# Kernel tuning notes

Hardware: AMD Instinct MI355X
Metric: run time of the kernel (lower is better)

Reference implementation:

```python
import jax, jax.numpy as jnp
import numpy as np

N = 100000   # nodes
E = 1600000  # edges (before self-loops)
F = 128      # num_features
H = 128      # hidden_dim
EPS = 1e-5   # BatchNorm eps


def setup_inputs() -> dict:
    key = jax.random.key(0)
    ks = jax.random.split(key, 8)
    x = jax.random.normal(ks[0], (N, F), dtype=jnp.float32)
    edge_index = jax.random.randint(ks[1], (2, E), 0, N, dtype=jnp.int64)

    def lin(k, din, dout):
        s = 1.0 / np.sqrt(din)
        kw, kb = jax.random.split(k)
        W = jax.random.uniform(kw, (din, dout), jnp.float32, -s, s)
        b = jax.random.uniform(kb, (dout,), jnp.float32, -s, s)
        return W, b

    W1, b1 = lin(ks[2], F, H)
    W2, b2 = lin(ks[3], H, H)
    W3, b3 = lin(ks[4], H, H)
    Wc, bc = lin(ks[5], H, 2)

    def bn_params():
        return (jnp.ones((H,), jnp.float32), jnp.zeros((H,), jnp.float32),
                jnp.zeros((H,), jnp.float32), jnp.ones((H,), jnp.float32))

    g1, be1, rm1, rv1 = bn_params()
    g2, be2, rm2, rv2 = bn_params()
    g3, be3, rm3, rv3 = bn_params()

    return {"x": x, "edge_index": edge_index,
            "W1": W1, "b1": b1, "W2": W2, "b2": b2, "W3": W3, "b3": b3,
            "g1": g1, "be1": be1, "rm1": rm1, "rv1": rv1,
            "g2": g2, "be2": be2, "rm2": rm2, "rv2": rv2,
            "g3": g3, "be3": be3, "rm3": rm3, "rv3": rv3,
            "Wc": Wc, "bc": bc}


def _gcn_norm(edge_index, num_nodes):
    # add self-loops, compute symmetric normalization (PyG GCNConv default)
    loop = jnp.arange(num_nodes, dtype=edge_index.dtype)
    src = jnp.concatenate([edge_index[0], loop])
    dst = jnp.concatenate([edge_index[1], loop])
    deg = jax.ops.segment_sum(jnp.ones_like(dst, dtype=jnp.float32), dst,
                              num_segments=num_nodes)
    dinv = jnp.where(deg > 0, jax.lax.rsqrt(deg), 0.0)
    norm = dinv[src] * dinv[dst]  # [E+N]
    return src, dst, norm


def _gcn_conv(x, W, b, src, dst, norm, num_nodes):
    h = x @ W                              # [N, H] linear first
    msg = h[src] * norm[:, None]           # gather + scale  [E+N, H]
    out = jax.ops.segment_sum(msg, dst, num_segments=num_nodes)  # scatter-add
    return out + b


def _bn_eval(x, g, be, rm, rv):
    return (x - rm) * jax.lax.rsqrt(rv + EPS) * g + be


def reference(x, edge_index,
              W1, b1, W2, b2, W3, b3,
              g1, be1, rm1, rv1,
              g2, be2, rm2, rv2,
              g3, be3, rm3, rv3,
              Wc, bc):
    n = x.shape[0]
    src, dst, norm = _gcn_norm(edge_index, n)
    h = _gcn_conv(x, W1, b1, src, dst, norm, n)
    h = _bn_eval(jax.nn.relu(h), g1, be1, rm1, rv1)
    # dropout: identity in eval mode
    h = _gcn_conv(h, W2, b2, src, dst, norm, n)
    h = _bn_eval(jax.nn.relu(h), g2, be2, rm2, rv2)
    h = _gcn_conv(h, W3, b3, src, dst, norm, n)
    h = _bn_eval(jax.nn.relu(h), g3, be3, rm3, rv3)
    return h @ Wc + bc  # [N, 2]
```

## Files before the change

kernel.cpp:

```cpp
#include <hip/hip_runtime.h>
#include <hip/hip_fp16.h>

#define BN_EPS 1e-5f
#define CHUNK 8192
#define BBITS 9

typedef _Float16 half8 __attribute__((ext_vector_type(8)));
typedef float f32x4 __attribute__((ext_vector_type(4)));

__device__ __forceinline__ float4 f4zero() { return make_float4(0.f, 0.f, 0.f, 0.f); }


__global__ __launch_bounds__(1024) void k_pack_hist(const float* __restrict__ W1,
                                                    const float* __restrict__ W2,
                                                    const float* __restrict__ W3,
                                                    _Float16* __restrict__ pW,
                                                    const int* __restrict__ dst,
                                                    int* __restrict__ tableT,
                                                    int nA, int nbuck, int e) {
    __shared__ int h[256];
    int tid = threadIdx.x;
    if (blockIdx.x < 6) {
        int t = blockIdx.x * 1024 + tid;
        int wi = t >> 11;
        int tt = t & 2047;
        const float* W = (wi == 0) ? W1 : ((wi == 1) ? W2 : W3);
        int kc = tt >> 9;
        int rem = tt & 511;
        int ct = rem >> 6;
        int lane = rem & 63;
        int q = lane >> 4;
        int col = ct * 16 + (lane & 15);
        half8 hh;
#pragma unroll
        for (int j = 0; j < 8; ++j)
            hh[j] = (_Float16)W[(kc * 32 + q * 8 + j) * 128 + col];
        *(half8*)(pW + (size_t)t * 8) = hh;
        return;
    }
    int blk = blockIdx.x - 6;
    if (tid < 256) h[tid] = 0;
    __syncthreads();
    int base = blk * CHUNK;
    if (base + CHUNK <= e) {
        const int4* d4 = (const int4*)(dst + base);
#pragma unroll
        for (int t = 0; t < CHUNK / 4096; ++t) {
            int4 d = d4[t * 1024 + tid];
            atomicAdd(&h[d.x >> BBITS], 1);
            atomicAdd(&h[d.y >> BBITS], 1);
            atomicAdd(&h[d.z >> BBITS], 1);
            atomicAdd(&h[d.w >> BBITS], 1);
        }
    } else {
        for (int i = base + tid; i < e; i += 1024)
            atomicAdd(&h[dst[i] >> BBITS], 1);
    }
    __syncthreads();
    for (int k = tid; k < nbuck; k += 1024)
        tableT[(size_t)k * nA + blk] = h[k];
}


__global__ __launch_bounds__(1024) void k_scan_block(const int* __restrict__ in,
                                                     int* __restrict__ outp,
                                                     int* __restrict__ partials, int len) {
    __shared__ int s[1024];
    int t = threadIdx.x;
    int gid = blockIdx.x * 1024 + t;
    int v = (gid < len) ? in[gid] : 0;
    int x = v;
    s[t] = x;
    __syncthreads();
    for (int d = 1; d < 1024; d <<= 1) {
        int y = (t >= d) ? s[t - d] : 0;
        __syncthreads();
        x += y;
        s[t] = x;
        __syncthreads();
    }
    if (gid < len) outp[gid] = x - v;
    if (t == 1023) partials[blockIdx.x] = x;
}

__global__ __launch_bounds__(256) void k_scan_addp(int* __restrict__ data,
                                                   const int* __restrict__ partials, int len) {
    __shared__ int red[256];
    int tid = threadIdx.x;
    int K = blockIdx.x >> 2;
    int s = 0;
    for (int t = tid; t < K; t += 256) s += partials[t];
    red[tid] = s;
    __syncthreads();
    for (int d = 128; d > 0; d >>= 1) {
        if (tid < d) red[tid] += red[tid + d];
        __syncthreads();
    }
    int gid = blockIdx.x * 256 + tid;
    if (gid < len) data[gid] += red[0];
}


__global__ __launch_bounds__(1024) void k_scatter(const int* __restrict__ src,
                                                  const int* __restrict__ dst,
                                                  const int* __restrict__ tableT,
                                                  int2* __restrict__ bed,
                                                  int nA, int nbuck, int e) {
    __shared__ int cur[256];
    int blk = blockIdx.x, tid = threadIdx.x;
    for (int k = tid; k < nbuck; k += 1024)
        cur[k] = tableT[(size_t)k * nA + blk];
    __syncthreads();
    int base = blk * CHUNK;
    if (base + CHUNK <= e) {
        const int4* s4 = (const int4*)(src + base);
        const int4* d4 = (const int4*)(dst + base);
#pragma unroll
        for (int t = 0; t < CHUNK / 4096; ++t) {
            int4 s = s4[t * 1024 + tid];
            int4 d = d4[t * 1024 + tid];
            int p0 = atomicAdd(&cur[d.x >> BBITS], 1); bed[p0] = make_int2(s.x, d.x);
            int p1 = atomicAdd(&cur[d.y >> BBITS], 1); bed[p1] = make_int2(s.y, d.y);
            int p2 = atomicAdd(&cur[d.z >> BBITS], 1); bed[p2] = make_int2(s.z, d.z);
            int p3 = atomicAdd(&cur[d.w >> BBITS], 1); bed[p3] = make_int2(s.w, d.w);
        }
    } else {
        for (int i = base + tid; i < e; i += 1024) {
            int d = dst[i];
            int p = atomicAdd(&cur[d >> BBITS], 1);
            bed[p] = make_int2(src[i], d);
        }
    }
}


template <bool AF32, bool SCALE>
__device__ __forceinline__ void gemm_body(int bid, int tid, char* smem,
                                          const void* __restrict__ Av,
                                          const _Float16* __restrict__ pW,
                                          const float* __restrict__ dinv,
                                          uint4* __restrict__ C, int n) {
    uint4* sW = (uint4*)smem;
    {
        const uint4* gW = (const uint4*)pW;
#pragma unroll
        for (int i = 0; i < 8; ++i) sW[tid + 256 * i] = gW[tid + 256 * i];
    }
    __syncthreads();

    int wave = tid >> 6, lane = tid & 63;
    int quad = lane >> 4, l16 = lane & 15;
    int row0 = bid * 64 + wave * 16;
    int arow = row0 + l16;
    int arowc = (arow < n) ? arow : (n - 1);

    half8 af[4];
    if (AF32) {
        const float* A = (const float*)Av + (size_t)arowc * 128 + quad * 8;
#pragma unroll
        for (int kc = 0; kc < 4; ++kc) {
            float4 lo = *(const float4*)(A + kc * 32);
            float4 hi = *(const float4*)(A + kc * 32 + 4);
            half8 h;
            h[0] = (_Float16)lo.x; h[1] = (_Float16)lo.y;
            h[2] = (_Float16)lo.z; h[3] = (_Float16)lo.w;
            h[4] = (_Float16)hi.x; h[5] = (_Float16)hi.y;
            h[6] = (_Float16)hi.z; h[7] = (_Float16)hi.w;
            af[kc] = h;
        }
    } else {
        const _Float16* A = (const _Float16*)Av + (size_t)arowc * 128 + quad * 8;
#pragma unroll
        for (int kc = 0; kc < 4; ++kc)
            af[kc] = *(const half8*)(A + kc * 32);
    }

    f32x4 acc[8];
#pragma unroll
    for (int ct = 0; ct < 8; ++ct) acc[ct] = (f32x4){0.f, 0.f, 0.f, 0.f};

#pragma unroll
    for (int kc = 0; kc < 4; ++kc) {
#pragma unroll
        for (int ct = 0; ct < 8; ++ct) {
            half8 bf = *(half8*)&sW[(kc * 8 + ct) * 64 + lane];
            acc[ct] = __builtin_amdgcn_mfma_f32_16x16x32_f16(af[kc], bf, acc[ct], 0, 0, 0);
        }
    }

    __syncthreads();

    _Float16* eb = (_Float16*)smem + wave * 16 * 136;
    float dv[4];
#pragma unroll
    for (int r = 0; r < 4; ++r) {
        if (SCALE) {
            int rr = row0 + quad * 4 + r;
            dv[r] = dinv[(rr < n) ? rr : (n - 1)];
        } else dv[r] = 1.f;
    }
#pragma unroll
    for (int ct = 0; ct < 8; ++ct)
#pragma unroll
        for (int r = 0; r < 4; ++r)
            eb[(quad * 4 + r) * 136 + ct * 16 + l16] =
                (_Float16)(SCALE ? acc[ct][r] * dv[r] : acc[ct][r]);

#pragma unroll
    for (int i = 0; i < 4; ++i) {
        int linear = i * 64 + lane;
        int r = linear >> 4, c = linear & 15;
        uint4 v = *(uint4*)((char*)eb + r * 272 + c * 16);
        int row = row0 + r;
        if (row < n) C[(size_t)row * 16 + c] = v;
    }
}

__global__ __launch_bounds__(256) void k_gemm_mfma(const void* __restrict__ Av,
                                                   const _Float16* __restrict__ pW,
                                                   const float* __restrict__ dinv,
                                                   uint4* __restrict__ C, int n) {
    __shared__ char smem[32768];
    gemm_body<false, true>(blockIdx.x, threadIdx.x, smem, Av, pW, dinv, C, n);
}


__global__ __launch_bounds__(256) void k_rank_gemm1(const int2* __restrict__ bed,
                                                    const int* __restrict__ tableT,
                                                    int2* __restrict__ offs2,
                                                    int* __restrict__ er,
                                                    float* __restrict__ dinv,
                                                    unsigned int* __restrict__ pad0,
                                                    const float* __restrict__ x,
                                                    const _Float16* __restrict__ pW,
                                                    uint4* __restrict__ C,
                                                    int nA, int nbuck, int n, int e) {
    __shared__ char smem[32768];
    int tid = threadIdx.x;
    int b = blockIdx.x;
    if (b >= nbuck) {
        gemm_body<true, false>(b - nbuck, tid, smem, x, pW, nullptr, C, n);
        return;
    }
    int* lcnt = (int*)smem;
    int* loff = lcnt + 512;
    int* s    = loff + 512;
    if (b == 0) {
        if (tid < 64) pad0[tid] = 0u;
        if (tid == 0) dinv[n] = 0.f;
    }
    for (int k = tid; k < 512; k += 256) lcnt[k] = 0;
    __syncthreads();
    int start = tableT[(size_t)b * nA];
    int end = (b + 1 < nbuck) ? tableT[(size_t)(b + 1) * nA] : e;
    for (int i = start + tid; i < end; i += 256)
        atomicAdd(&lcnt[bed[i].y & 511], 1);
    __syncthreads();
    int t2 = tid * 2;
    int c0 = lcnt[t2], c1 = lcnt[t2 + 1];
    int p0 = (c0 + 7) & ~7, p1 = (c1 + 7) & ~7;
    int xsum = p0 + p1;
    s[tid] = xsum;
    __syncthreads();
    for (int d = 1; d < 256; d <<= 1) {
        int y = (tid >= d) ? s[tid - d] : 0;
        __syncthreads();
        xsum += y;
        s[tid] = xsum;
        __syncthreads();
    }
    int ebase = start + (b << 12);
    int base0 = xsum - p0 - p1;
    loff[t2] = base0;
    loff[t2 + 1] = base0 + p0;
    {
        int node = (b << BBITS) + t2;
        if (node < n) {
            int o = ebase + base0;
            offs2[node] = make_int2(o, o + p0);
            dinv[node] = rsqrtf((float)(c0 + 1));
            for (int j = c0; j < p0; ++j) er[o + j] = n << 8;
        }
        node = (b << BBITS) + t2 + 1;
        if (node < n) {
            int o = ebase + base0 + p0;
            offs2[node] = make_int2(o, o + p1);
            dinv[node] = rsqrtf((float)(c1 + 1));
            for (int j = c1; j < p1; ++j) er[o + j] = n << 8;
        }
    }
    __syncthreads();
    for (int k = tid; k < 512; k += 256) lcnt[k] = 0;
    __syncthreads();
    for (int i = start + tid; i < end; i += 256) {
        int2 q = bed[i];
        int l = q.y & 511;
        int r = atomicAdd(&lcnt[l], 1);
        er[ebase + loff[l] + r] = q.x << 8;
    }
}


__device__ __forceinline__ void acc_row4(float4& aL, float4& aH, uint4 q) {
    asm("v_fma_mix_f32 %0, %1, 1.0, %0 op_sel:[0,0,0] op_sel_hi:[1,0,0]" : "+v"(aL.x) : "v"(q.x));
    asm("v_fma_mix_f32 %0, %1, 1.0, %0 op_sel:[1,0,0] op_sel_hi:[1,0,0]" : "+v"(aL.y) : "v"(q.x));
    asm("v_fma_mix_f32 %0, %1, 1.0, %0 op_sel:[0,0,0] op_sel_hi:[1,0,0]" : "+v"(aL.z) : "v"(q.y));
    asm("v_fma_mix_f32 %0, %1, 1.0, %0 op_sel:[1,0,0] op_sel_hi:[1,0,0]" : "+v"(aL.w) : "v"(q.y));
    asm("v_fma_mix_f32 %0, %1, 1.0, %0 op_sel:[0,0,0] op_sel_hi:[1,0,0]" : "+v"(aH.x) : "v"(q.z));
    asm("v_fma_mix_f32 %0, %1, 1.0, %0 op_sel:[1,0,0] op_sel_hi:[1,0,0]" : "+v"(aH.y) : "v"(q.z));
    asm("v_fma_mix_f32 %0, %1, 1.0, %0 op_sel:[0,0,0] op_sel_hi:[1,0,0]" : "+v"(aH.z) : "v"(q.w));
    asm("v_fma_mix_f32 %0, %1, 1.0, %0 op_sel:[1,0,0] op_sel_hi:[1,0,0]" : "+v"(aH.w) : "v"(q.w));
}

__device__ __forceinline__ void acc_row4s(float4& aL, float4& aH, uint4 q, float s) {
    asm("v_fma_mix_f32 %0, %1, %2, %0 op_sel:[0,0,0] op_sel_hi:[1,0,0]" : "+v"(aL.x) : "v"(q.x), "v"(s));
    asm("v_fma_mix_f32 %0, %1, %2, %0 op_sel:[1,0,0] op_sel_hi:[1,0,0]" : "+v"(aL.y) : "v"(q.x), "v"(s));
    asm("v_fma_mix_f32 %0, %1, %2, %0 op_sel:[0,0,0] op_sel_hi:[1,0,0]" : "+v"(aL.z) : "v"(q.y), "v"(s));
    asm("v_fma_mix_f32 %0, %1, %2, %0 op_sel:[1,0,0] op_sel_hi:[1,0,0]" : "+v"(aL.w) : "v"(q.y), "v"(s));
    asm("v_fma_mix_f32 %0, %1, %2, %0 op_sel:[0,0,0] op_sel_hi:[1,0,0]" : "+v"(aH.x) : "v"(q.z), "v"(s));
    asm("v_fma_mix_f32 %0, %1, %2, %0 op_sel:[1,0,0] op_sel_hi:[1,0,0]" : "+v"(aH.y) : "v"(q.z), "v"(s));
    asm("v_fma_mix_f32 %0, %1, %2, %0 op_sel:[0,0,0] op_sel_hi:[1,0,0]" : "+v"(aH.z) : "v"(q.w), "v"(s));
    asm("v_fma_mix_f32 %0, %1, %2, %0 op_sel:[1,0,0] op_sel_hi:[1,0,0]" : "+v"(aH.w) : "v"(q.w), "v"(s));
}


template <bool FUSE_CLS, bool SRC_SCALE>
__global__ __launch_bounds__(256) void k_aggregate(const uint4* __restrict__ Ah,
                                                   const int2* __restrict__ offs2,
                                                   const int* __restrict__ er,
                                                   const float* __restrict__ dinv,
                                                   const float* __restrict__ bias,
                                                   const float* __restrict__ g,
                                                   const float* __restrict__ be,
                                                   const float* __restrict__ rm,
                                                   const float* __restrict__ rv,
                                                   uint4* __restrict__ Hout,
                                                   const float* __restrict__ Wc,
                                                   const float* __restrict__ bc,
                                                   float* __restrict__ out, int n) {
    int lane = threadIdx.x & 15;
    int node = blockIdx.x * 16 + (threadIdx.x >> 4);
    if (node >= n) return;

    const char* AhB = (const char*)Ah;
    unsigned int l16b = (unsigned int)lane * 16u;

    float di = dinv[node];
    float4 aL = f4zero(), aH = f4zero();
    {
        uint4 qs = *(const uint4*)(AhB + (((unsigned int)node << 8) + l16b));
        if (SRC_SCALE) acc_row4s(aL, aH, qs, di);
        else           acc_row4(aL, aH, qs);
    }

    int2 offc = offs2[node];
    for (int e = offc.x; e < offc.y; e += 8) {
        int4 ra = *(const int4*)(er + e);
        int4 rb = *(const int4*)(er + e + 4);
        uint4 v0 = *(const uint4*)(AhB + ((unsigned int)ra.x + l16b));
        uint4 v1 = *(const uint4*)(AhB + ((unsigned int)ra.y + l16b));
        uint4 v2 = *(const uint4*)(AhB + ((unsigned int)ra.z + l16b));
        uint4 v3 = *(const uint4*)(AhB + ((unsigned int)ra.w + l16b));
        uint4 v4 = *(const uint4*)(AhB + ((unsigned int)rb.x + l16b));
        uint4 v5 = *(const uint4*)(AhB + ((unsigned int)rb.y + l16b));
        uint4 v6 = *(const uint4*)(AhB + ((unsigned int)rb.z + l16b));
        uint4 v7 = *(const uint4*)(AhB + ((unsigned int)rb.w + l16b));
        if (SRC_SCALE) {
            float d0 = dinv[(unsigned int)ra.x >> 8];
            float d1 = dinv[(unsigned int)ra.y >> 8];
            float d2 = dinv[(unsigned int)ra.z >> 8];
            float d3 = dinv[(unsigned int)ra.w >> 8];
            float d4 = dinv[(unsigned int)rb.x >> 8];
            float d5 = dinv[(unsigned int)rb.y >> 8];
            float d6 = dinv[(unsigned int)rb.z >> 8];
            float d7 = dinv[(unsigned int)rb.w >> 8];
            acc_row4s(aL, aH, v0, d0); acc_row4s(aL, aH, v1, d1);
            acc_row4s(aL, aH, v2, d2); acc_row4s(aL, aH, v3, d3);
            acc_row4s(aL, aH, v4, d4); acc_row4s(aL, aH, v5, d5);
            acc_row4s(aL, aH, v6, d6); acc_row4s(aL, aH, v7, d7);
        } else {
            acc_row4(aL, aH, v0); acc_row4(aL, aH, v1); acc_row4(aL, aH, v2); acc_row4(aL, aH, v3);
            acc_row4(aL, aH, v4); acc_row4(aL, aH, v5); acc_row4(aL, aH, v6); acc_row4(aL, aH, v7);
        }
    }

    aL.x *= di; aL.y *= di; aL.z *= di; aL.w *= di;
    aH.x *= di; aH.y *= di; aH.z *= di; aH.w *= di;

    float4 bL  = ((const float4*)bias)[2 * lane], bH  = ((const float4*)bias)[2 * lane + 1];
    float4 gL  = ((const float4*)g)[2 * lane],    gH  = ((const float4*)g)[2 * lane + 1];
    float4 beL = ((const float4*)be)[2 * lane],   beH = ((const float4*)be)[2 * lane + 1];
    float4 rmL = ((const float4*)rm)[2 * lane],   rmH = ((const float4*)rm)[2 * lane + 1];
    float4 rvL = ((const float4*)rv)[2 * lane],   rvH = ((const float4*)rv)[2 * lane + 1];

    float4 oL, oH;
    float v;
    v = fmaxf(aL.x + bL.x, 0.f); oL.x = (v - rmL.x) * rsqrtf(rvL.x + BN_EPS) * gL.x + beL.x;
    v = fmaxf(aL.y + bL.y, 0.f); oL.y = (v - rmL.y) * rsqrtf(rvL.y + BN_EPS) * gL.y + beL.y;
    v = fmaxf(aL.z + bL.z, 0.f); oL.z = (v - rmL.z) * rsqrtf(rvL.z + BN_EPS) * gL.z + beL.z;
    v = fmaxf(aL.w + bL.w, 0.f); oL.w = (v - rmL.w) * rsqrtf(rvL.w + BN_EPS) * gL.w + beL.w;
    v = fmaxf(aH.x + bH.x, 0.f); oH.x = (v - rmH.x) * rsqrtf(rvH.x + BN_EPS) * gH.x + beH.x;
    v = fmaxf(aH.y + bH.y, 0.f); oH.y = (v - rmH.y) * rsqrtf(rvH.y + BN_EPS) * gH.y + beH.y;
    v = fmaxf(aH.z + bH.z, 0.f); oH.z = (v - rmH.z) * rsqrtf(rvH.z + BN_EPS) * gH.z + beH.z;
    v = fmaxf(aH.w + bH.w, 0.f); oH.w = (v - rmH.w) * rsqrtf(rvH.w + BN_EPS) * gH.w + beH.w;

    if (!FUSE_CLS) {
        __half2 p0 = __floats2half2_rn(oL.x, oL.y);
        __half2 p1 = __floats2half2_rn(oL.z, oL.w);
        __half2 p2 = __floats2half2_rn(oH.x, oH.y);
        __half2 p3 = __floats2half2_rn(oH.z, oH.w);
        uint4 u;
        u.x = *(unsigned int*)&p0;
        u.y = *(unsigned int*)&p1;
        u.z = *(unsigned int*)&p2;
        u.w = *(unsigned int*)&p3;
        Hout[(size_t)node * 16 + lane] = u;
    } else {
        const float4* Wv = (const float4*)Wc;
        float4 w0 = Wv[4 * lane];
        float4 w1 = Wv[4 * lane + 1];
        float4 w2 = Wv[4 * lane + 2];
        float4 w3 = Wv[4 * lane + 3];
        float p0 = oL.x * w0.x + oL.y * w0.z + oL.z * w1.x + oL.w * w1.z
                 + oH.x * w2.x + oH.y * w2.z + oH.z * w3.x + oH.w * w3.z;
        float p1 = oL.x * w0.y + oL.y * w0.w + oL.z * w1.y + oL.w * w1.w
                 + oH.x * w2.y + oH.y * w2.w + oH.z * w3.y + oH.w * w3.w;
#pragma unroll
        for (int d = 8; d >= 1; d >>= 1) {
            p0 += __shfl_down(p0, d, 16);
            p1 += __shfl_down(p1, d, 16);
        }
        if (lane == 0) {
            out[node * 2 + 0] = p0 + bc[0];
            out[node * 2 + 1] = p1 + bc[1];
        }
    }
}


extern "C" void kernel_launch(void* const* d_in, const int* in_sizes, int n_in,
                              void* d_out, int out_size, void* d_ws, size_t ws_size,
                              hipStream_t stream) {
    const float* x   = (const float*)d_in[0];
    const int*   ei  = (const int*)d_in[1];
    const float* W1  = (const float*)d_in[2];
    const float* b1  = (const float*)d_in[3];
    const float* W2  = (const float*)d_in[4];
    const float* b2  = (const float*)d_in[5];
    const float* W3  = (const float*)d_in[6];
    const float* b3  = (const float*)d_in[7];
    const float* g1  = (const float*)d_in[8];
    const float* be1 = (const float*)d_in[9];
    const float* rm1 = (const float*)d_in[10];
    const float* rv1 = (const float*)d_in[11];
    const float* g2  = (const float*)d_in[12];
    const float* be2 = (const float*)d_in[13];
    const float* rm2 = (const float*)d_in[14];
    const float* rv2 = (const float*)d_in[15];
    const float* g3  = (const float*)d_in[16];
    const float* be3 = (const float*)d_in[17];
    const float* rm3 = (const float*)d_in[18];
    const float* rv3 = (const float*)d_in[19];
    const float* Wc  = (const float*)d_in[20];
    const float* bc  = (const float*)d_in[21];
    float* out = (float*)d_out;

    int n = in_sizes[0] / 128;
    int e = in_sizes[1] / 2;
    const int* src = ei;
    const int* dst = ei + e;

    char* ws = (char*)d_ws;
    size_t off = 0;
    auto alloc = [&](size_t bytes) -> char* {
        char* p = ws + off;
        off += (bytes + 255) & ~(size_t)255;
        return p;
    };
    int nA    = (e + CHUNK - 1) / CHUNK;
    int nbuck = (n + (1 << BBITS) - 1) >> BBITS;
    int tlen  = nbuck * nA;
    int erCap = e + (nbuck << 12) + 64;

    char*      buf0     = (char*) alloc((size_t)(n + 1) * 256);
    char*      buf1     = (char*) alloc((size_t)(n + 1) * 256);
    float*     dinv     = (float*)alloc((size_t)(n + 1) * 4);
    int2*      offs2    = (int2*) alloc((size_t)n * 8);
    int*       tableT   = (int*)  alloc((size_t)(tlen + 1) * 4);
    int*       parts    = (int*)  alloc(8192);
    int*       er       = (int*)  alloc((size_t)erCap * 4);
    _Float16*  pW       = (_Float16*)alloc(3 * 16384 * 2);
    (void)ws_size; (void)n_in; (void)out_size;

    int2* bed = (int2*)buf1;

    int nbT   = (tlen + 1023) / 1024;
    int gT    = (tlen + 255) / 256;
    int gGemm = (n + 63) / 64;
    int gAgg  = (n + 15) / 16;

    k_pack_hist<<<6 + nA, 1024, 0, stream>>>(W1, W2, W3, pW, dst, tableT, nA, nbuck, e);
    k_scan_block<<<nbT, 1024, 0, stream>>>(tableT, tableT, parts, tlen);
    k_scan_addp<<<gT, 256, 0, stream>>>(tableT, parts, tlen);
    k_scatter<<<nA, 1024, 0, stream>>>(src, dst, tableT, bed, nA, nbuck, e);
    k_rank_gemm1<<<nbuck + gGemm, 256, 0, stream>>>(
        bed, tableT, offs2, er, dinv,
        (unsigned int*)(buf0 + (size_t)n * 256),
        x, pW, (uint4*)buf0, nA, nbuck, n, e);

    k_aggregate<false, true><<<gAgg, 256, 0, stream>>>(
        (const uint4*)buf0, offs2, er, dinv, b1, g1, be1, rm1, rv1,
        (uint4*)buf1, nullptr, nullptr, nullptr, n);
    k_gemm_mfma<<<gGemm, 256, 0, stream>>>(buf1, pW + 16384, dinv, (uint4*)buf0, n);
    k_aggregate<false, false><<<gAgg, 256, 0, stream>>>(
        (const uint4*)buf0, offs2, er, dinv, b2, g2, be2, rm2, rv2,
        (uint4*)buf1, nullptr, nullptr, nullptr, n);
    k_gemm_mfma<<<gGemm, 256, 0, stream>>>(buf1, pW + 32768, dinv, (uint4*)buf0, n);
    k_aggregate<true, false><<<gAgg, 256, 0, stream>>>(
        (const uint4*)buf0, offs2, er, dinv, b3, g3, be3, rm3, rv3,
        nullptr, Wc, bc, out, n);
}
```

Baseline: 374.0 us.

## Move first GEMM into histogram kernel, widen rank blocks, prefetch edge indices

Moves the first-layer GEMM (converting W1 from fp32 in shared memory) out of the rank kernel and into the histogram kernel, so it runs alongside histogram and weight packing instead of competing with the serial rank step. The histogram now uses smaller 2048-edge chunks in 256-thread blocks to raise parallelism, and the scatter reads every fourth table column to keep its 8192-edge chunks. The rank kernel runs with 1024 threads and a 512-wide scan. The aggregation loop software-prefetches the next group of edge indices. The risks are a larger prefix table to scan and extra per-block W1 conversion work.

Result: slower. 388.5 us (+3.9%).

```diff
diff --git a/kernel.cpp b/kernel.cpp
--- a/kernel.cpp
+++ b/kernel.cpp
@@ -2,7 +2,8 @@
 #include <hip/hip_fp16.h>
 
 #define BN_EPS 1e-5f
-#define CHUNK 8192
+#define HCHUNK 2048
+#define SCHUNK 8192
 #define BBITS 9
 
 typedef _Float16 half8 __attribute__((ext_vector_type(8)));
@@ -11,54 +12,159 @@
 __device__ __forceinline__ float4 f4zero() { return make_float4(0.f, 0.f, 0.f, 0.f); }
 
 
-__global__ __launch_bounds__(1024) void k_pack_hist(const float* __restrict__ W1,
+template <bool AF32, bool WF32, bool SCALE>
+__device__ __forceinline__ void gemm_body(int bid, int tid, char* smem,
+                                          const void* __restrict__ Av,
+                                          const void* __restrict__ Wv_,
+                                          const float* __restrict__ dinv,
+                                          uint4* __restrict__ C, int n) {
+    uint4* sW = (uint4*)smem;
+    if (WF32) {
+        const float* Wf = (const float*)Wv_;
+#pragma unroll
+        for (int i = 0; i < 8; ++i) {
+            int t = tid + 256 * i;
+            int kc = t >> 9, rem = t & 511;
+            int ct = rem >> 6, lane = rem & 63;
+            int q = lane >> 4, col = ct * 16 + (lane & 15);
+            half8 hh;
+#pragma unroll
+            for (int j = 0; j < 8; ++j)
+                hh[j] = (_Float16)Wf[(kc * 32 + q * 8 + j) * 128 + col];
+            ((half8*)sW)[t] = hh;
+        }
+    } else {
+        const uint4* gW = (const uint4*)Wv_;
+#pragma unroll
+        for (int i = 0; i < 8; ++i) sW[tid + 256 * i] = gW[tid + 256 * i];
+    }
+    __syncthreads();
+
+    int wave = tid >> 6, lane = tid & 63;
+    int quad = lane >> 4, l16 = lane & 15;
+    int row0 = bid * 64 + wave * 16;
+    int arow = row0 + l16;
+    int arowc = (arow < n) ? arow : (n - 1);
+
+    half8 af[4];
+    if (AF32) {
+        const float* A = (const float*)Av + (size_t)arowc * 128 + quad * 8;
+#pragma unroll
+        for (int kc = 0; kc < 4; ++kc) {
+            float4 lo = *(const float4*)(A + kc * 32);
+            float4 hi = *(const float4*)(A + kc * 32 + 4);
+            half8 h;
+            h[0] = (_Float16)lo.x; h[1] = (_Float16)lo.y;
+            h[2] = (_Float16)lo.z; h[3] = (_Float16)lo.w;
+            h[4] = (_Float16)hi.x; h[5] = (_Float16)hi.y;
+            h[6] = (_Float16)hi.z; h[7] = (_Float16)hi.w;
+            af[kc] = h;
+        }
+    } else {
+        const _Float16* A = (const _Float16*)Av + (size_t)arowc * 128 + quad * 8;
+#pragma unroll
+        for (int kc = 0; kc < 4; ++kc)
+            af[kc] = *(const half8*)(A + kc * 32);
+    }
+
+    f32x4 acc[8];
+#pragma unroll
+    for (int ct = 0; ct < 8; ++ct) acc[ct] = (f32x4){0.f, 0.f, 0.f, 0.f};
+
+#pragma unroll
+    for (int kc = 0; kc < 4; ++kc) {
+#pragma unroll
+        for (int ct = 0; ct < 8; ++ct) {
+            half8 bf = *(half8*)&sW[(kc * 8 + ct) * 64 + lane];
+            acc[ct] = __builtin_amdgcn_mfma_f32_16x16x32_f16(af[kc], bf, acc[ct], 0, 0, 0);
+        }
+    }
+
+    __syncthreads();
+
+    _Float16* eb = (_Float16*)smem + wave * 16 * 136;
+    float dv[4];
+#pragma unroll
+    for (int r = 0; r < 4; ++r) {
+        if (SCALE) {
+            int rr = row0 + quad * 4 + r;
+            dv[r] = dinv[(rr < n) ? rr : (n - 1)];
+        } else dv[r] = 1.f;
+    }
+#pragma unroll
+    for (int ct = 0; ct < 8; ++ct)
+#pragma unroll
+        for (int r = 0; r < 4; ++r)
+            eb[(quad * 4 + r) * 136 + ct * 16 + l16] =
+                (_Float16)(SCALE ? acc[ct][r] * dv[r] : acc[ct][r]);
+
+#pragma unroll
+    for (int i = 0; i < 4; ++i) {
+        int linear = i * 64 + lane;
+        int r = linear >> 4, c = linear & 15;
+        uint4 v = *(uint4*)((char*)eb + r * 272 + c * 16);
+        int row = row0 + r;
+        if (row < n) C[(size_t)row * 16 + c] = v;
+    }
+}
+
+
+__global__ __launch_bounds__(256) void k_hist_gemm1(const int* __restrict__ dst,
+                                                    int* __restrict__ tableT,
+                                                    int nA2, int nbuck, int e,
+                                                    const float* __restrict__ x,
+                                                    const float* __restrict__ W1,
                                                     const float* __restrict__ W2,
                                                     const float* __restrict__ W3,
                                                     _Float16* __restrict__ pW,
-                                                    const int* __restrict__ dst,
-                                                    int* __restrict__ tableT,
-                                                    int nA, int nbuck, int e) {
-    __shared__ int h[256];
+                                                    uint4* __restrict__ C,
+                                                    int n, int gGemm) {
+    __shared__ char smem[32768];
     int tid = threadIdx.x;
-    if (blockIdx.x < 6) {
-        int t = blockIdx.x * 1024 + tid;
-        int wi = t >> 11;
-        int tt = t & 2047;
-        const float* W = (wi == 0) ? W1 : ((wi == 1) ? W2 : W3);
-        int kc = tt >> 9;
-        int rem = tt & 511;
-        int ct = rem >> 6;
-        int lane = rem & 63;
-        int q = lane >> 4;
-        int col = ct * 16 + (lane & 15);
-        half8 hh;
-#pragma unroll
-        for (int j = 0; j < 8; ++j)
-            hh[j] = (_Float16)W[(kc * 32 + q * 8 + j) * 128 + col];
-        *(half8*)(pW + (size_t)t * 8) = hh;
+    int b = blockIdx.x;
+    if (b < nA2) {
+        int* h = (int*)smem;
+        h[tid] = 0;
+        __syncthreads();
+        int base = b * HCHUNK;
+        if (base + HCHUNK <= e) {
+            const int4* d4 = (const int4*)(dst + base);
+            int4 d0 = d4[tid];
+            int4 d1 = d4[tid + 256];
+            atomicAdd(&h[d0.x >> BBITS], 1);
+            atomicAdd(&h[d0.y >> BBITS], 1);
+            atomicAdd(&h[d0.z >> BBITS], 1);
+            atomicAdd(&h[d0.w >> BBITS], 1);
+            atomicAdd(&h[d1.x >> BBITS], 1);
+            atomicAdd(&h[d1.y >> BBITS], 1);
+            atomicAdd(&h[d1.z >> BBITS], 1);
+            atomicAdd(&h[d1.w >> BBITS], 1);
+        } else {
+            for (int i = base + tid; i < e; i += 256)
+                atomicAdd(&h[dst[i] >> BBITS], 1);
+        }
+        __syncthreads();
+        for (int k = tid; k < nbuck; k += 256)
+            tableT[(size_t)k * nA2 + b] = h[k];
         return;
     }
-    int blk = blockIdx.x - 6;
-    if (tid < 256) h[tid] = 0;
-    __syncthreads();
-    int base = blk * CHUNK;
-    if (base + CHUNK <= e) {
-        const int4* d4 = (const int4*)(dst + base);
-#pragma unroll
-        for (int t = 0; t < CHUNK / 4096; ++t) {
-            int4 d = d4[t * 1024 + tid];
-            atomicAdd(&h[d.x >> BBITS], 1);
-            atomicAdd(&h[d.y >> BBITS], 1);
-            atomicAdd(&h[d.z >> BBITS], 1);
-            atomicAdd(&h[d.w >> BBITS], 1);
-        }
-    } else {
-        for (int i = base + tid; i < e; i += 1024)
-            atomicAdd(&h[dst[i] >> BBITS], 1);
-    }
-    __syncthreads();
-    for (int k = tid; k < nbuck; k += 1024)
-        tableT[(size_t)k * nA + blk] = h[k];
+    b -= nA2;
+    if (b < gGemm) {
+        gemm_body<true, true, false>(b, tid, smem, x, W1, nullptr, C, n);
+        return;
+    }
+    int t = (b - gGemm) * 256 + tid;
+    int wi = t >> 11;
+    const float* W = wi ? W3 : W2;
+    int tt = t & 2047;
+    int kc = tt >> 9, rem = tt & 511;
+    int ct = rem >> 6, lane = rem & 63;
+    int q = lane >> 4, col = ct * 16 + (lane & 15);
+    half8 hh;
+#pragma unroll
+    for (int j = 0; j < 8; ++j)
+        hh[j] = (_Float16)W[(kc * 32 + q * 8 + j) * 128 + col];
+    *(half8*)(pW + 16384 + (size_t)t * 8) = hh;
 }
 
 
@@ -105,18 +211,18 @@
                                                   const int* __restrict__ dst,
                                                   const int* __restrict__ tableT,
                                                   int2* __restrict__ bed,
-                                                  int nA, int nbuck, int e) {
+                                                  int nA2, int nbuck, int e) {
     __shared__ int cur[256];
     int blk = blockIdx.x, tid = threadIdx.x;
     for (int k = tid; k < nbuck; k += 1024)
-        cur[k] = tableT[(size_t)k * nA + blk];
-    __syncthreads();
-    int base = blk * CHUNK;
-    if (base + CHUNK <= e) {
+        cur[k] = tableT[(size_t)k * nA2 + blk * 4];
+    __syncthreads();
+    int base = blk * SCHUNK;
+    if (base + SCHUNK <= e) {
         const int4* s4 = (const int4*)(src + base);
         const int4* d4 = (const int4*)(dst + base);
 #pragma unroll
-        for (int t = 0; t < CHUNK / 4096; ++t) {
+        for (int t = 0; t < SCHUNK / 4096; ++t) {
             int4 s = s4[t * 1024 + tid];
             int4 d = d4[t * 1024 + tid];
             int p0 = atomicAdd(&cur[d.x >> BBITS], 1); bed[p0] = make_int2(s.x, d.x);
@@ -134,165 +240,56 @@
 }
 
 
-template <bool AF32, bool SCALE>
-__device__ __forceinline__ void gemm_body(int bid, int tid, char* smem,
-                                          const void* __restrict__ Av,
-                                          const _Float16* __restrict__ pW,
-                                          const float* __restrict__ dinv,
-                                          uint4* __restrict__ C, int n) {
-    uint4* sW = (uint4*)smem;
-    {
-        const uint4* gW = (const uint4*)pW;
-#pragma unroll
-        for (int i = 0; i < 8; ++i) sW[tid + 256 * i] = gW[tid + 256 * i];
-    }
-    __syncthreads();
-
-    int wave = tid >> 6, lane = tid & 63;
-    int quad = lane >> 4, l16 = lane & 15;
-    int row0 = bid * 64 + wave * 16;
-    int arow = row0 + l16;
-    int arowc = (arow < n) ? arow : (n - 1);
-
-    half8 af[4];
-    if (AF32) {
-        const float* A = (const float*)Av + (size_t)arowc * 128 + quad * 8;
-#pragma unroll
-        for (int kc = 0; kc < 4; ++kc) {
-            float4 lo = *(const float4*)(A + kc * 32);
-            float4 hi = *(const float4*)(A + kc * 32 + 4);
-            half8 h;
-            h[0] = (_Float16)lo.x; h[1] = (_Float16)lo.y;
-            h[2] = (_Float16)lo.z; h[3] = (_Float16)lo.w;
-            h[4] = (_Float16)hi.x; h[5] = (_Float16)hi.y;
-            h[6] = (_Float16)hi.z; h[7] = (_Float16)hi.w;
-            af[kc] = h;
-        }
-    } else {
-        const _Float16* A = (const _Float16*)Av + (size_t)arowc * 128 + quad * 8;
-#pragma unroll
-        for (int kc = 0; kc < 4; ++kc)
-            af[kc] = *(const half8*)(A + kc * 32);
-    }
-
-    f32x4 acc[8];
-#pragma unroll
-    for (int ct = 0; ct < 8; ++ct) acc[ct] = (f32x4){0.f, 0.f, 0.f, 0.f};
-
-#pragma unroll
-    for (int kc = 0; kc < 4; ++kc) {
-#pragma unroll
-        for (int ct = 0; ct < 8; ++ct) {
-            half8 bf = *(half8*)&sW[(kc * 8 + ct) * 64 + lane];
-            acc[ct] = __builtin_amdgcn_mfma_f32_16x16x32_f16(af[kc], bf, acc[ct], 0, 0, 0);
-        }
-    }
-
-    __syncthreads();
-
-    _Float16* eb = (_Float16*)smem + wave * 16 * 136;
-    float dv[4];
-#pragma unroll
-    for (int r = 0; r < 4; ++r) {
-        if (SCALE) {
-            int rr = row0 + quad * 4 + r;
-            dv[r] = dinv[(rr < n) ? rr : (n - 1)];
-        } else dv[r] = 1.f;
-    }
-#pragma unroll
-    for (int ct = 0; ct < 8; ++ct)
-#pragma unroll
-        for (int r = 0; r < 4; ++r)
-            eb[(quad * 4 + r) * 136 + ct * 16 + l16] =
-                (_Float16)(SCALE ? acc[ct][r] * dv[r] : acc[ct][r]);
-
-#pragma unroll
-    for (int i = 0; i < 4; ++i) {
-        int linear = i * 64 + lane;
-        int r = linear >> 4, c = linear & 15;
-        uint4 v = *(uint4*)((char*)eb + r * 272 + c * 16);
-        int row = row0 + r;
-        if (row < n) C[(size_t)row * 16 + c] = v;
-    }
-}
-
-__global__ __launch_bounds__(256) void k_gemm_mfma(const void* __restrict__ Av,
-                                                   const _Float16* __restrict__ pW,
-                                                   const float* __restrict__ dinv,
-                                                   uint4* __restrict__ C, int n) {
-    __shared__ char smem[32768];
-    gemm_body<false, true>(blockIdx.x, threadIdx.x, smem, Av, pW, dinv, C, n);
-}
-
-
-__global__ __launch_bounds__(256) void k_rank_gemm1(const int2* __restrict__ bed,
-                                                    const int* __restrict__ tableT,
-                                                    int2* __restrict__ offs2,
-                                                    int* __restrict__ er,
-                                                    float* __restrict__ dinv,
-                                                    unsigned int* __restrict__ pad0,
-                                                    const float* __restrict__ x,
-                                                    const _Float16* __restrict__ pW,
-                                                    uint4* __restrict__ C,
-                                                    int nA, int nbuck, int n, int e) {
-    __shared__ char smem[32768];
-    int tid = threadIdx.x;
-    int b = blockIdx.x;
-    if (b >= nbuck) {
-        gemm_body<true, false>(b - nbuck, tid, smem, x, pW, nullptr, C, n);
-        return;
-    }
-    int* lcnt = (int*)smem;
-    int* loff = lcnt + 512;
-    int* s    = loff + 512;
+__global__ __launch_bounds__(1024) void k_rank(const int2* __restrict__ bed,
+                                               const int* __restrict__ tableT,
+                                               int2* __restrict__ offs2,
+                                               int* __restrict__ er,
+                                               float* __restrict__ dinv,
+                                               unsigned int* __restrict__ pad0,
+                                               int nA2, int nbuck, int n, int e) {
+    __shared__ int lcnt[512];
+    __shared__ int loff[512];
+    __shared__ int s[512];
+    int tid = threadIdx.x, b = blockIdx.x;
     if (b == 0) {
         if (tid < 64) pad0[tid] = 0u;
         if (tid == 0) dinv[n] = 0.f;
     }
-    for (int k = tid; k < 512; k += 256) lcnt[k] = 0;
-    __syncthreads();
-    int start = tableT[(size_t)b * nA];
-    int end = (b + 1 < nbuck) ? tableT[(size_t)(b + 1) * nA] : e;
-    for (int i = start + tid; i < end; i += 256)
+    if (tid < 512) lcnt[tid] = 0;
+    __syncthreads();
+    int start = tableT[(size_t)b * nA2];
+    int end = (b + 1 < nbuck) ? tableT[(size_t)(b + 1) * nA2] : e;
+    for (int i = start + tid; i < end; i += 1024)
         atomicAdd(&lcnt[bed[i].y & 511], 1);
     __syncthreads();
-    int t2 = tid * 2;
-    int c0 = lcnt[t2], c1 = lcnt[t2 + 1];
-    int p0 = (c0 + 7) & ~7, p1 = (c1 + 7) & ~7;
-    int xsum = p0 + p1;
-    s[tid] = xsum;
-    __syncthreads();
-    for (int d = 1; d < 256; d <<= 1) {
-        int y = (tid >= d) ? s[tid - d] : 0;
-        __syncthreads();
-        xsum += y;
-        s[tid] = xsum;
+    int c = 0, p = 0, x = 0;
+    if (tid < 512) {
+        c = lcnt[tid];
+        p = (c + 7) & ~7;
+        x = p;
+        s[tid] = x;
+    }
+    __syncthreads();
+    for (int d = 1; d < 512; d <<= 1) {
+        int y = (tid < 512 && tid >= d) ? s[tid - d] : 0;
+        __syncthreads();
+        if (tid < 512) { x += y; s[tid] = x; }
         __syncthreads();
     }
     int ebase = start + (b << 12);
-    int base0 = xsum - p0 - p1;
-    loff[t2] = base0;
-    loff[t2 + 1] = base0 + p0;
-    {
-        int node = (b << BBITS) + t2;
+    if (tid < 512) {
+        loff[tid] = x - p;
+        int node = (b << BBITS) + tid;
         if (node < n) {
-            int o = ebase + base0;
-            offs2[node] = make_int2(o, o + p0);
-            dinv[node] = rsqrtf((float)(c0 + 1));
-            for (int j = c0; j < p0; ++j) er[o + j] = n << 8;
-        }
-        node = (b << BBITS) + t2 + 1;
-        if (node < n) {
-            int o = ebase + base0 + p0;
-            offs2[node] = make_int2(o, o + p1);
-            dinv[node] = rsqrtf((float)(c1 + 1));
-            for (int j = c1; j < p1; ++j) er[o + j] = n << 8;
-        }
-    }
-    __syncthreads();
-    for (int k = tid; k < 512; k += 256) lcnt[k] = 0;
-    __syncthreads();
-    for (int i = start + tid; i < end; i += 256) {
+            int o = ebase + x - p;
+            offs2[node] = make_int2(o, o + p);
+            dinv[node] = rsqrtf((float)(c + 1));
+            for (int j = c; j < p; ++j) er[o + j] = n << 8;
+        }
+        lcnt[tid] = 0;
+    }
+    __syncthreads();
+    for (int i = start + tid; i < end; i += 1024) {
         int2 q = bed[i];
         int l = q.y & 511;
         int r = atomicAdd(&lcnt[l], 1);
@@ -354,9 +351,18 @@
     }
 
     int2 offc = offs2[node];
-    for (int e = offc.x; e < offc.y; e += 8) {
-        int4 ra = *(const int4*)(er + e);
-        int4 rb = *(const int4*)(er + e + 4);
+    int e0 = offc.x, e1 = offc.y;
+    int4 ra = make_int4(0, 0, 0, 0), rb = make_int4(0, 0, 0, 0);
+    if (e0 < e1) {
+        ra = *(const int4*)(er + e0);
+        rb = *(const int4*)(er + e0 + 4);
+    }
+    for (int ee = e0; ee < e1; ee += 8) {
+        int4 ran = ra, rbn = rb;
+        if (ee + 8 < e1) {
+            ran = *(const int4*)(er + ee + 8);
+            rbn = *(const int4*)(er + ee + 12);
+        }
         uint4 v0 = *(const uint4*)(AhB + ((unsigned int)ra.x + l16b));
         uint4 v1 = *(const uint4*)(AhB + ((unsigned int)ra.y + l16b));
         uint4 v2 = *(const uint4*)(AhB + ((unsigned int)ra.z + l16b));
@@ -382,6 +388,7 @@
             acc_row4(aL, aH, v0); acc_row4(aL, aH, v1); acc_row4(aL, aH, v2); acc_row4(aL, aH, v3);
             acc_row4(aL, aH, v4); acc_row4(aL, aH, v5); acc_row4(aL, aH, v6); acc_row4(aL, aH, v7);
         }
+        ra = ran; rb = rbn;
     }
 
     aL.x *= di; aL.y *= di; aL.z *= di; aL.w *= di;
@@ -435,6 +442,15 @@
             out[node * 2 + 1] = p1 + bc[1];
         }
     }
+}
+
+
+__global__ __launch_bounds__(256) void k_gemm_mfma(const void* __restrict__ Av,
+                                                   const _Float16* __restrict__ pW,
+                                                   const float* __restrict__ dinv,
+                                                   uint4* __restrict__ C, int n) {
+    __shared__ char smem[32768];
+    gemm_body<false, false, true>(blockIdx.x, threadIdx.x, smem, Av, pW, dinv, C, n);
 }
 
 
@@ -477,9 +493,10 @@
         off += (bytes + 255) & ~(size_t)255;
         return p;
     };
-    int nA    = (e + CHUNK - 1) / CHUNK;
+    int nA2   = (e + HCHUNK - 1) / HCHUNK;
+    int nS    = (e + SCHUNK - 1) / SCHUNK;
     int nbuck = (n + (1 << BBITS) - 1) >> BBITS;
-    int tlen  = nbuck * nA;
+    int tlen  = nbuck * nA2;
     int erCap = e + (nbuck << 12) + 64;
 
     char*      buf0     = (char*) alloc((size_t)(n + 1) * 256);
@@ -499,14 +516,14 @@
     int gGemm = (n + 63) / 64;
     int gAgg  = (n + 15) / 16;
 
-    k_pack_hist<<<6 + nA, 1024, 0, stream>>>(W1, W2, W3, pW, dst, tableT, nA, nbuck, e);
+    k_hist_gemm1<<<nA2 + gGemm + 16, 256, 0, stream>>>(
+        dst, tableT, nA2, nbuck, e, x, W1, W2, W3, pW, (uint4*)buf0, n, gGemm);
     k_scan_block<<<nbT, 1024, 0, stream>>>(tableT, tableT, parts, tlen);
     k_scan_addp<<<gT, 256, 0, stream>>>(tableT, parts, tlen);
-    k_scatter<<<nA, 1024, 0, stream>>>(src, dst, tableT, bed, nA, nbuck, e);
-    k_rank_gemm1<<<nbuck + gGemm, 256, 0, stream>>>(
-        bed, tableT, offs2, er, dinv,
-        (unsigned int*)(buf0 + (size_t)n * 256),
-        x, pW, (uint4*)buf0, nA, nbuck, n, e);
+    k_scatter<<<nS, 1024, 0, stream>>>(src, dst, tableT, bed, nA2, nbuck, e);
+    k_rank<<<nbuck, 1024, 0, stream>>>(bed, tableT, offs2, er, dinv,
+                                       (unsigned int*)(buf0 + (size_t)n * 256),
+                                       nA2, nbuck, n, e);
 
     k_aggregate<false, true><<<gAgg, 256, 0, stream>>>(
         (const uint4*)buf0, offs2, er, dinv, b1, g1, be1, rm1, rv1,
```
